# Performance work log

Hardware: AMD Instinct MI355X
Metric: run time of the kernel (lower is better)

Reference implementation:

```python
import jax, jax.numpy as jnp
import numpy as np

N = 50000          # number of parent nodes / neighborhoods
D_IN = 256         # input_size
K = 8              # points decoded per neighborhood
GLOBAL_DIMS = [256, 128, 64]
FC_DIMS = [256, 256, 256]


def _linear_params(key, d_in, d_out):
    kw, kb = jax.random.split(key)
    W = jax.random.normal(kw, (d_in, d_out), dtype=jnp.float32) * 0.05
    b = jax.random.normal(kb, (d_out,), dtype=jnp.float32) * 0.05
    return W, b


def setup_inputs() -> dict:
    key = jax.random.key(0)
    keys = jax.random.split(key, 8)
    inp = {"input_features": jax.random.normal(keys[0], (N, D_IN), dtype=jnp.float32)}
    # global MLP: 256 -> 256 -> 128 -> 64
    d = D_IN
    for i, nb in enumerate(GLOBAL_DIMS):
        W, b = _linear_params(keys[1 + i], d, nb)
        inp[f"Wg{i}"], inp[f"bg{i}"] = W, b
        d = nb
    # neighborhood decoder head: 64 -> K*3
    inp["Wdec"], inp["bdec"] = _linear_params(keys[4], GLOBAL_DIMS[-1], K * 3)
    # per-point MLP: (256 + 64 + 3) -> 256 -> 256 -> 256
    d = D_IN + GLOBAL_DIMS[-1] + 3
    for i, nb in enumerate(FC_DIMS):
        W, b = _linear_params(keys[5 + i], d, nb)
        inp[f"W{i}"], inp[f"b{i}"] = W, b
        d = nb
    return inp


def reference(input_features, Wg0, bg0, Wg1, bg1, Wg2, bg2, Wdec, bdec,
              W0, b0, W1, b1, W2, b2):
    relu = jax.nn.relu
    # global feature MLP on node features: [N, 256] -> [N, 64]
    feats = input_features
    for W, b in ((Wg0, bg0), (Wg1, bg1), (Wg2, bg2)):
        feats = relu(feats @ W + b)
    # neighborhood decoder: K relative 3D points per node -> [N*K, 3]
    relative_points = (feats @ Wdec + bdec).reshape(-1, 3)
    cluster = jnp.repeat(jnp.arange(N, dtype=jnp.int32), K)  # [N*K]
    # gather (duplicate) parent features per decoded point
    nbr_dup = jnp.take(feats, cluster, axis=0)               # [N*K, 64]
    inp_dup = jnp.take(input_features, cluster, axis=0)      # [N*K, 256]
    decoded = jnp.concatenate([inp_dup, nbr_dup, relative_points], axis=1)  # [N*K, 323]
    for W, b in ((W0, b0), (W1, b1), (W2, b2)):
        decoded = relu(decoded @ W + b)
    return relative_points, decoded, cluster
```

## Files before the change

kernel.cpp:

```cpp
#include <hip/hip_runtime.h>
#include <hip/hip_bf16.h>

typedef __attribute__((ext_vector_type(8))) __bf16 bf16x8;
typedef __attribute__((ext_vector_type(4))) float f32x4;
typedef __attribute__((ext_vector_type(4))) unsigned short u16x4;

#define NN 50000
#define TM1 16
#define PNODES 16

#define FEATS_OFF 212992
#define GW_OFF    3412992

__device__ __forceinline__ unsigned short f2bf(float f) {
    unsigned int u = __builtin_bit_cast(unsigned int, f);
    u = (u + 0x7FFFu + ((u >> 16) & 1u)) >> 16;
    return (unsigned short)u;
}
__device__ __forceinline__ float bf2f(unsigned short h) {
    return __builtin_bit_cast(float, (unsigned int)h << 16);
}

__global__ __launch_bounds__(256) void k_prep(
    const float* __restrict__ W0, const float* __restrict__ W1,
    const float* __restrict__ W2,
    const float* __restrict__ Wg0, const float* __restrict__ Wg1,
    const float* __restrict__ Wg2,
    unsigned short* __restrict__ wbf)
{
    int idx = blockIdx.x * 256 + threadIdx.x;
    if (idx < 81920) {
        int n = idx / 320, k = idx - n * 320;
        wbf[idx] = f2bf(W0[(size_t)k * 256 + n]);
    } else if (idx < 147456) {
        int e = idx - 81920;
        int n = e >> 8, k = e & 255;
        wbf[idx] = f2bf(W1[(size_t)k * 256 + n]);
    } else if (idx < 212992) {
        int e = idx - 147456;
        int n = e >> 8, k = e & 255;
        wbf[idx] = f2bf(W2[(size_t)k * 256 + n]);
    } else if (idx < 319488) {
        int e = idx - 212992;
        float v; int oh, ol;
        if (e < 65536) {
            int n = e >> 8, k = e & 255;
            v = Wg0[(size_t)k * 256 + n];
            oh = GW_OFF + e; ol = GW_OFF + 65536 + e;
        } else if (e < 98304) {
            int e2 = e - 65536;
            int n = e2 >> 8, k = e2 & 255;
            v = Wg1[(size_t)k * 128 + n];
            oh = GW_OFF + 131072 + e2; ol = GW_OFF + 163840 + e2;
        } else {
            int e3 = e - 98304;
            int n = e3 >> 7, k = e3 & 127;
            v = Wg2[(size_t)k * 64 + n];
            oh = GW_OFF + 196608 + e3; ol = GW_OFF + 204800 + e3;
        }
        unsigned short h = f2bf(v);
        wbf[oh] = h;
        wbf[ol] = f2bf(v - bf2f(h));
    }
}

__global__ __launch_bounds__(256, 4) void k_global(
    const float* __restrict__ x,
    const float* __restrict__ bg0, const float* __restrict__ bg1,
    const float* __restrict__ bg2,
    const float* __restrict__ Wdec, const float* __restrict__ bdec,
    const unsigned short* __restrict__ gw,
    unsigned short* __restrict__ feats_bf,
    float* __restrict__ out_rel,
    float* __restrict__ out_cluster)
{
    __shared__ __attribute__((aligned(16))) unsigned char smem[37888];
    unsigned short* xh  = (unsigned short*)(smem);
    unsigned short* xl  = (unsigned short*)(smem + 8448);
    unsigned short* q1h = (unsigned short*)(smem);
    unsigned short* q1l = (unsigned short*)(smem + 4352);
    unsigned short* hh  = (unsigned short*)(smem + 16896);
    unsigned short* hl  = (unsigned short*)(smem + 25344);
    float*          g2  = (float*)(smem + 33792);

    const int tid  = threadIdx.x;
    const int lane = tid & 63;
    const int w    = tid >> 6;
    const int quad = lane >> 4;
    const int l15  = lane & 15;
    const int blk  = blockIdx.x;

    {
        const float4* xg = (const float4*)(x + (size_t)blk * TM1 * 256);
        #pragma unroll
        for (int it = 0; it < 4; ++it) {
            int e = tid + it * 256;
            int r = e >> 6, c4 = e & 63;
            float4 v = xg[e];
            u16x4 hv, lv;
            hv[0] = f2bf(v.x); lv[0] = f2bf(v.x - bf2f(hv[0]));
            hv[1] = f2bf(v.y); lv[1] = f2bf(v.y - bf2f(hv[1]));
            hv[2] = f2bf(v.z); lv[2] = f2bf(v.z - bf2f(hv[2]));
            hv[3] = f2bf(v.w); lv[3] = f2bf(v.w - bf2f(hv[3]));
            *(u16x4*)&xh[r * 264 + c4 * 4] = hv;
            *(u16x4*)&xl[r * 264 + c4 * 4] = lv;
        }
    }
    __syncthreads();

    {
        const unsigned short* Wh = gw;
        const unsigned short* Wl = gw + 65536;
        f32x4 acc[4];
        f32x4 z = {0.f, 0.f, 0.f, 0.f};
        #pragma unroll
        for (int t = 0; t < 4; ++t) acc[t] = z;
        for (int ks = 0; ks < 8; ++ks) {
            int k0 = ks * 32 + quad * 8;
            bf16x8 ah = *(const bf16x8*)&xh[l15 * 264 + k0];
            bf16x8 al = *(const bf16x8*)&xl[l15 * 264 + k0];
            #pragma unroll
            for (int t = 0; t < 4; ++t) {
                int n = w * 64 + t * 16 + l15;
                bf16x8 bh = *(const bf16x8*)(Wh + (size_t)n * 256 + k0);
                bf16x8 bl = *(const bf16x8*)(Wl + (size_t)n * 256 + k0);
                acc[t] = __builtin_amdgcn_mfma_f32_16x16x32_bf16(ah, bh, acc[t], 0, 0, 0);
                acc[t] = __builtin_amdgcn_mfma_f32_16x16x32_bf16(al, bh, acc[t], 0, 0, 0);
                acc[t] = __builtin_amdgcn_mfma_f32_16x16x32_bf16(ah, bl, acc[t], 0, 0, 0);
            }
        }
        #pragma unroll
        for (int t = 0; t < 4; ++t) {
            int col = w * 64 + t * 16 + l15;
            float bb = bg0[col];
            #pragma unroll
            for (int r = 0; r < 4; ++r) {
                int row = quad * 4 + r;
                float v = fmaxf(acc[t][r] + bb, 0.f);
                unsigned short h = f2bf(v);
                hh[row * 264 + col] = h;
                hl[row * 264 + col] = f2bf(v - bf2f(h));
            }
        }
    }
    __syncthreads();

    {
        const unsigned short* Wh = gw + 131072;
        const unsigned short* Wl = gw + 163840;
        f32x4 acc[2];
        f32x4 z = {0.f, 0.f, 0.f, 0.f};
        acc[0] = z; acc[1] = z;
        for (int ks = 0; ks < 8; ++ks) {
            int k0 = ks * 32 + quad * 8;
            bf16x8 ah = *(const bf16x8*)&hh[l15 * 264 + k0];
            bf16x8 al = *(const bf16x8*)&hl[l15 * 264 + k0];
            #pragma unroll
            for (int t = 0; t < 2; ++t) {
                int n = w * 32 + t * 16 + l15;
                bf16x8 bh = *(const bf16x8*)(Wh + (size_t)n * 256 + k0);
                bf16x8 bl = *(const bf16x8*)(Wl + (size_t)n * 256 + k0);
                acc[t] = __builtin_amdgcn_mfma_f32_16x16x32_bf16(ah, bh, acc[t], 0, 0, 0);
                acc[t] = __builtin_amdgcn_mfma_f32_16x16x32_bf16(al, bh, acc[t], 0, 0, 0);
                acc[t] = __builtin_amdgcn_mfma_f32_16x16x32_bf16(ah, bl, acc[t], 0, 0, 0);
            }
        }
        #pragma unroll
        for (int t = 0; t < 2; ++t) {
            int col = w * 32 + t * 16 + l15;
            float bb = bg1[col];
            #pragma unroll
            for (int r = 0; r < 4; ++r) {
                int row = quad * 4 + r;
                float v = fmaxf(acc[t][r] + bb, 0.f);
                unsigned short h = f2bf(v);
                q1h[row * 136 + col] = h;
                q1l[row * 136 + col] = f2bf(v - bf2f(h));
            }
        }
    }
    __syncthreads();

    {
        const unsigned short* Wh = gw + 196608;
        const unsigned short* Wl = gw + 204800;
        f32x4 acc = {0.f, 0.f, 0.f, 0.f};
        for (int ks = 0; ks < 4; ++ks) {
            int k0 = ks * 32 + quad * 8;
            bf16x8 ah = *(const bf16x8*)&q1h[l15 * 136 + k0];
            bf16x8 al = *(const bf16x8*)&q1l[l15 * 136 + k0];
            int n = w * 16 + l15;
            bf16x8 bh = *(const bf16x8*)(Wh + (size_t)n * 128 + k0);
            bf16x8 bl = *(const bf16x8*)(Wl + (size_t)n * 128 + k0);
            acc = __builtin_amdgcn_mfma_f32_16x16x32_bf16(ah, bh, acc, 0, 0, 0);
            acc = __builtin_amdgcn_mfma_f32_16x16x32_bf16(al, bh, acc, 0, 0, 0);
            acc = __builtin_amdgcn_mfma_f32_16x16x32_bf16(ah, bl, acc, 0, 0, 0);
        }
        int col = w * 16 + l15;
        float bb = bg2[col];
        #pragma unroll
        for (int r = 0; r < 4; ++r) {
            int row = quad * 4 + r;
            g2[row * 64 + col] = fmaxf(acc[r] + bb, 0.f);
        }
    }
    __syncthreads();

    {
        const float* src = g2 + tid * 4;
        u16x4 p;
        p[0] = f2bf(src[0]); p[1] = f2bf(src[1]);
        p[2] = f2bf(src[2]); p[3] = f2bf(src[3]);
        *(u16x4*)&feats_bf[(size_t)blk * (TM1 * 64) + tid * 4] = p;
    }

    for (int tt = tid; tt < TM1 * 24; tt += 256) {
        int m = tt / 24;
        int c = tt - m * 24;
        float acc = bdec[c];
        for (int i = 0; i < 64; ++i) acc += g2[m * 64 + i] * Wdec[i * 24 + c];
        out_rel[(size_t)blk * (TM1 * 24) + tt] = acc;
    }

    if (tid < TM1 * 8) {
        out_cluster[(size_t)blk * (TM1 * 8) + tid] = (float)(blk * TM1 + (tid >> 3));
    }
}

__global__ __launch_bounds__(512, 4) void k_points(
    const float* __restrict__ x,
    const unsigned short* __restrict__ feats_bf,
    const float* __restrict__ rel_in,
    const unsigned short* __restrict__ wbf,
    const float* __restrict__ W0f,
    const float* __restrict__ b0,
    const float* __restrict__ b1,
    const float* __restrict__ b2,
    float* __restrict__ out_dec)
{
    __shared__ __attribute__((aligned(16))) unsigned char smem[70144];
    unsigned char*  hB   = smem;
    unsigned short* xcat = (unsigned short*)smem;
    float*          sp   = (float*)(smem + 49152);
    float*          w3   = (float*)(smem + 65536);
    float*          rl   = (float*)(smem + 68608);

    const int tid  = threadIdx.x;
    const int lane = tid & 63;
    const int w    = tid >> 6;
    const int wr   = w >> 2;
    const int wc   = w & 3;
    const int quad = lane >> 4;
    const int l15  = lane & 15;
    const int blk  = blockIdx.x;
    const size_t nb = (size_t)blk * PNODES;

    {
        const float4* xg = (const float4*)(x + nb * 256);
        #pragma unroll
        for (int it = 0; it < 2; ++it) {
            int e = tid + it * 512;
            int r = e >> 6, c4 = e & 63;
            float4 v = xg[e];
            u16x4 hv;
            hv[0] = f2bf(v.x); hv[1] = f2bf(v.y);
            hv[2] = f2bf(v.z); hv[3] = f2bf(v.w);
            *(u16x4*)&xcat[r * 336 + c4 * 4] = hv;
        }
        {
            int e = tid * 2;
            int r = e >> 6, c = e & 63;
            *(unsigned int*)&xcat[r * 336 + 256 + c] =
                *(const unsigned int*)&feats_bf[nb * 64 + e];
        }
        for (int e = tid; e < 768; e += 512)
            w3[e] = W0f[(size_t)(320 + (e >> 8)) * 256 + (e & 255)];
        if (tid < 384) rl[tid] = rel_in[nb * 24 + tid];
    }
    __syncthreads();

    {
        const unsigned short* W0t = wbf;
        f32x4 acc[2];
        f32x4 z = {0.f, 0.f, 0.f, 0.f};
        acc[0] = z; acc[1] = z;
        for (int ks = 0; ks < 10; ++ks) {
            int k0 = ks * 32 + quad * 8;
            bf16x8 a = *(const bf16x8*)&xcat[l15 * 336 + k0];
            #pragma unroll
            for (int t = 0; t < 2; ++t) {
                int n = w * 32 + t * 16 + l15;
                bf16x8 b = *(const bf16x8*)(W0t + (size_t)n * 320 + k0);
                acc[t] = __builtin_amdgcn_mfma_f32_16x16x32_bf16(a, b, acc[t], 0, 0, 0);
            }
        }
        #pragma unroll
        for (int t = 0; t < 2; ++t) {
            int col = w * 32 + t * 16 + l15;
            float bb = b0[col];
            #pragma unroll
            for (int r = 0; r < 4; ++r) {
                int row = quad * 4 + r;
                sp[row * 256 + col] = acc[t][r] + bb;
            }
        }
    }
    __syncthreads();

    {
        float4 sv0 = *(const float4*)&sp[(2 * w) * 256 + lane * 4];
        float4 sv1 = *(const float4*)&sp[(2 * w + 1) * 256 + lane * 4];
        float4 wa  = *(const float4*)&w3[lane * 4];
        float4 wb4 = *(const float4*)&w3[256 + lane * 4];
        float4 wc4 = *(const float4*)&w3[512 + lane * 4];
        __syncthreads();
        #pragma unroll
        for (int it = 0; it < 16; ++it) {
            int row  = w * 16 + it;
            int node = 2 * w + (it >> 3);
            int p    = it & 7;
            float4 sv = (it < 8) ? sv0 : sv1;
            float ra = rl[node * 24 + p * 3 + 0];
            float rb = rl[node * 24 + p * 3 + 1];
            float rc = rl[node * 24 + p * 3 + 2];
            float v0 = fmaxf(sv.x + ra * wa.x + rb * wb4.x + rc * wc4.x, 0.f);
            float v1 = fmaxf(sv.y + ra * wa.y + rb * wb4.y + rc * wc4.y, 0.f);
            float v2 = fmaxf(sv.z + ra * wa.z + rb * wb4.z + rc * wc4.z, 0.f);
            float v3 = fmaxf(sv.w + ra * wa.w + rb * wb4.w + rc * wc4.w, 0.f);
            unsigned int lo = (unsigned int)f2bf(v0) | ((unsigned int)f2bf(v1) << 16);
            unsigned int hi = (unsigned int)f2bf(v2) | ((unsigned int)f2bf(v3) << 16);
            uint2 pk; pk.x = lo; pk.y = hi;
            int byteoff = row * 512 +
                ((((lane >> 1) ^ (row & 7)) << 4) | ((lane & 1) << 3));
            *(uint2*)(hB + byteoff) = pk;
        }
    }
    __syncthreads();

    {
        const unsigned short* W1t = wbf + 81920;
        f32x4 acc[4][4];
        f32x4 z = {0.f, 0.f, 0.f, 0.f};
        #pragma unroll
        for (int m = 0; m < 4; ++m)
            #pragma unroll
            for (int t = 0; t < 4; ++t) acc[m][t] = z;
        for (int ks = 0; ks < 8; ++ks) {
            int k0 = ks * 32 + quad * 8;
            int g  = k0 >> 3;
            bf16x8 a[4], b[4];
            #pragma unroll
            for (int m = 0; m < 4; ++m) {
                int row = wr * 64 + m * 16 + l15;
                a[m] = *(const bf16x8*)(hB + row * 512 + ((g ^ (row & 7)) << 4));
            }
            #pragma unroll
            for (int t = 0; t < 4; ++t)
                b[t] = *(const bf16x8*)(W1t + (size_t)(wc * 64 + t * 16 + l15) * 256 + k0);
            #pragma unroll
            for (int m = 0; m < 4; ++m)
                #pragma unroll
                for (int t = 0; t < 4; ++t)
                    acc[m][t] = __builtin_amdgcn_mfma_f32_16x16x32_bf16(a[m], b[t], acc[m][t], 0, 0, 0);
        }
        __syncthreads();
        #pragma unroll
        for (int t = 0; t < 4; ++t) {
            int col = wc * 64 + t * 16 + l15;
            float bb = b1[col];
            #pragma unroll
            for (int m = 0; m < 4; ++m) {
                #pragma unroll
                for (int r = 0; r < 4; ++r) {
                    int row = wr * 64 + m * 16 + quad * 4 + r;
                    int byteoff = row * 512 +
                        ((((col >> 3) ^ (row & 7)) << 4) | ((col & 7) << 1));
                    *(unsigned short*)(hB + byteoff) =
                        f2bf(fmaxf(acc[m][t][r] + bb, 0.f));
                }
            }
        }
    }
    __syncthreads();

    {
        const unsigned short* W2t = wbf + 147456;
        f32x4 acc[4][4];
        f32x4 z = {0.f, 0.f, 0.f, 0.f};
        #pragma unroll
        for (int m = 0; m < 4; ++m)
            #pragma unroll
            for (int t = 0; t < 4; ++t) acc[m][t] = z;
        for (int ks = 0; ks < 8; ++ks) {
            int k0 = ks * 32 + quad * 8;
            int g  = k0 >> 3;
            bf16x8 a[4], b[4];
            #pragma unroll
            for (int m = 0; m < 4; ++m) {
                int row = wr * 64 + m * 16 + l15;
                a[m] = *(const bf16x8*)(hB + row * 512 + ((g ^ (row & 7)) << 4));
            }
            #pragma unroll
            for (int t = 0; t < 4; ++t)
                b[t] = *(const bf16x8*)(W2t + (size_t)(wc * 64 + t * 16 + l15) * 256 + k0);
            #pragma unroll
            for (int m = 0; m < 4; ++m)
                #pragma unroll
                for (int t = 0; t < 4; ++t)
                    acc[m][t] = __builtin_amdgcn_mfma_f32_16x16x32_bf16(a[m], b[t], acc[m][t], 0, 0, 0);
        }
        #pragma unroll
        for (int t = 0; t < 4; ++t) {
            int col = wc * 64 + t * 16 + l15;
            float bb = b2[col];
            #pragma unroll
            for (int m = 0; m < 4; ++m) {
                #pragma unroll
                for (int r = 0; r < 4; ++r) {
                    int row = wr * 64 + m * 16 + quad * 4 + r;
                    out_dec[((size_t)blk * 128 + row) * 256 + col] =
                        fmaxf(acc[m][t][r] + bb, 0.f);
                }
            }
        }
    }
}

extern "C" void kernel_launch(void* const* d_in, const int* in_sizes, int n_in,
                              void* d_out, int out_size, void* d_ws, size_t ws_size,
                              hipStream_t stream) {
    const float* x    = (const float*)d_in[0];
    const float* Wg0  = (const float*)d_in[1];
    const float* bg0  = (const float*)d_in[2];
    const float* Wg1  = (const float*)d_in[3];
    const float* bg1  = (const float*)d_in[4];
    const float* Wg2  = (const float*)d_in[5];
    const float* bg2  = (const float*)d_in[6];
    const float* Wdec = (const float*)d_in[7];
    const float* bdec = (const float*)d_in[8];
    const float* W0   = (const float*)d_in[9];
    const float* b0   = (const float*)d_in[10];
    const float* W1   = (const float*)d_in[11];
    const float* b1   = (const float*)d_in[12];
    const float* W2   = (const float*)d_in[13];
    const float* b2   = (const float*)d_in[14];

    float* out      = (float*)d_out;
    float* out_rel  = out;
    float* out_dec  = out + 1200000;
    float* out_clu  = out + 103600000;

    unsigned short* wbf      = (unsigned short*)d_ws;
    unsigned short* feats_bf = wbf + FEATS_OFF;
    unsigned short* gw       = wbf + GW_OFF;

    k_prep<<<1248, 256, 0, stream>>>(W0, W1, W2, Wg0, Wg1, Wg2, wbf);
    k_global<<<NN / TM1, 256, 0, stream>>>(x, bg0, bg1, bg2, Wdec, bdec, gw,
                                           feats_bf, out_rel, out_clu);
    k_points<<<NN / PNODES, 512, 0, stream>>>(x, feats_bf, out_rel,
                                              wbf, W0, b0, b1, b2, out_dec);
}
```

Baseline: 878.6 us.

## Halve node tiles per block and stage decoder output through LDS for coalesced stores

```diff
diff --git a/kernel.cpp b/kernel.cpp
--- a/kernel.cpp
+++ b/kernel.cpp
@@ -6,8 +6,8 @@
 typedef __attribute__((ext_vector_type(4))) unsigned short u16x4;
 
 #define NN 50000
-#define TM1 16
-#define PNODES 16
+#define GNODES 8
+#define PNODES 8
 
 #define FEATS_OFF 212992
 #define GW_OFF    3412992
@@ -64,7 +64,7 @@
     }
 }
 
-__global__ __launch_bounds__(256, 4) void k_global(
+__global__ __launch_bounds__(256, 6) void k_global(
     const float* __restrict__ x,
     const float* __restrict__ bg0, const float* __restrict__ bg1,
     const float* __restrict__ bg2,
@@ -74,14 +74,14 @@
     float* __restrict__ out_rel,
     float* __restrict__ out_cluster)
 {
-    __shared__ __attribute__((aligned(16))) unsigned char smem[37888];
+    __shared__ __attribute__((aligned(16))) unsigned char smem[18944];
     unsigned short* xh  = (unsigned short*)(smem);
-    unsigned short* xl  = (unsigned short*)(smem + 8448);
+    unsigned short* xl  = (unsigned short*)(smem + 4224);
     unsigned short* q1h = (unsigned short*)(smem);
-    unsigned short* q1l = (unsigned short*)(smem + 4352);
-    unsigned short* hh  = (unsigned short*)(smem + 16896);
-    unsigned short* hl  = (unsigned short*)(smem + 25344);
-    float*          g2  = (float*)(smem + 33792);
+    unsigned short* q1l = (unsigned short*)(smem + 2176);
+    unsigned short* gh  = (unsigned short*)(smem + 8448);
+    unsigned short* gl  = (unsigned short*)(smem + 12672);
+    float*          g2  = (float*)(smem + 16896);
 
     const int tid  = threadIdx.x;
     const int lane = tid & 63;
@@ -89,11 +89,12 @@
     const int quad = lane >> 4;
     const int l15  = lane & 15;
     const int blk  = blockIdx.x;
-
-    {
-        const float4* xg = (const float4*)(x + (size_t)blk * TM1 * 256);
-        #pragma unroll
-        for (int it = 0; it < 4; ++it) {
+    const size_t nb = (size_t)blk * GNODES;
+
+    {
+        const float4* xg = (const float4*)(x + nb * 256);
+        #pragma unroll
+        for (int it = 0; it < 2; ++it) {
             int e = tid + it * 256;
             int r = e >> 6, c4 = e & 63;
             float4 v = xg[e];
@@ -115,10 +116,11 @@
         f32x4 z = {0.f, 0.f, 0.f, 0.f};
         #pragma unroll
         for (int t = 0; t < 4; ++t) acc[t] = z;
+        const int ar = (l15 & 7) * 264;
         for (int ks = 0; ks < 8; ++ks) {
             int k0 = ks * 32 + quad * 8;
-            bf16x8 ah = *(const bf16x8*)&xh[l15 * 264 + k0];
-            bf16x8 al = *(const bf16x8*)&xl[l15 * 264 + k0];
+            bf16x8 ah = *(const bf16x8*)&xh[ar + k0];
+            bf16x8 al = *(const bf16x8*)&xl[ar + k0];
             #pragma unroll
             for (int t = 0; t < 4; ++t) {
                 int n = w * 64 + t * 16 + l15;
@@ -136,10 +138,12 @@
             #pragma unroll
             for (int r = 0; r < 4; ++r) {
                 int row = quad * 4 + r;
-                float v = fmaxf(acc[t][r] + bb, 0.f);
-                unsigned short h = f2bf(v);
-                hh[row * 264 + col] = h;
-                hl[row * 264 + col] = f2bf(v - bf2f(h));
+                if (row < 8) {
+                    float v = fmaxf(acc[t][r] + bb, 0.f);
+                    unsigned short hv = f2bf(v);
+                    gh[row * 264 + col] = hv;
+                    gl[row * 264 + col] = f2bf(v - bf2f(hv));
+                }
             }
         }
     }
@@ -151,10 +155,11 @@
         f32x4 acc[2];
         f32x4 z = {0.f, 0.f, 0.f, 0.f};
         acc[0] = z; acc[1] = z;
+        const int ar = (l15 & 7) * 264;
         for (int ks = 0; ks < 8; ++ks) {
             int k0 = ks * 32 + quad * 8;
-            bf16x8 ah = *(const bf16x8*)&hh[l15 * 264 + k0];
-            bf16x8 al = *(const bf16x8*)&hl[l15 * 264 + k0];
+            bf16x8 ah = *(const bf16x8*)&gh[ar + k0];
+            bf16x8 al = *(const bf16x8*)&gl[ar + k0];
             #pragma unroll
             for (int t = 0; t < 2; ++t) {
                 int n = w * 32 + t * 16 + l15;
@@ -172,10 +177,12 @@
             #pragma unroll
             for (int r = 0; r < 4; ++r) {
                 int row = quad * 4 + r;
-                float v = fmaxf(acc[t][r] + bb, 0.f);
-                unsigned short h = f2bf(v);
-                q1h[row * 136 + col] = h;
-                q1l[row * 136 + col] = f2bf(v - bf2f(h));
+                if (row < 8) {
+                    float v = fmaxf(acc[t][r] + bb, 0.f);
+                    unsigned short hv = f2bf(v);
+                    q1h[row * 136 + col] = hv;
+                    q1l[row * 136 + col] = f2bf(v - bf2f(hv));
+                }
             }
         }
     }
@@ -185,10 +192,11 @@
         const unsigned short* Wh = gw + 196608;
         const unsigned short* Wl = gw + 204800;
         f32x4 acc = {0.f, 0.f, 0.f, 0.f};
+        const int ar = (l15 & 7) * 136;
         for (int ks = 0; ks < 4; ++ks) {
             int k0 = ks * 32 + quad * 8;
-            bf16x8 ah = *(const bf16x8*)&q1h[l15 * 136 + k0];
-            bf16x8 al = *(const bf16x8*)&q1l[l15 * 136 + k0];
+            bf16x8 ah = *(const bf16x8*)&q1h[ar + k0];
+            bf16x8 al = *(const bf16x8*)&q1l[ar + k0];
             int n = w * 16 + l15;
             bf16x8 bh = *(const bf16x8*)(Wh + (size_t)n * 128 + k0);
             bf16x8 bl = *(const bf16x8*)(Wl + (size_t)n * 128 + k0);
@@ -201,33 +209,31 @@
         #pragma unroll
         for (int r = 0; r < 4; ++r) {
             int row = quad * 4 + r;
-            g2[row * 64 + col] = fmaxf(acc[r] + bb, 0.f);
-        }
-    }
-    __syncthreads();
-
-    {
+            if (row < 8) g2[row * 64 + col] = fmaxf(acc[r] + bb, 0.f);
+        }
+    }
+    __syncthreads();
+
+    if (tid < 128) {
         const float* src = g2 + tid * 4;
         u16x4 p;
         p[0] = f2bf(src[0]); p[1] = f2bf(src[1]);
         p[2] = f2bf(src[2]); p[3] = f2bf(src[3]);
-        *(u16x4*)&feats_bf[(size_t)blk * (TM1 * 64) + tid * 4] = p;
-    }
-
-    for (int tt = tid; tt < TM1 * 24; tt += 256) {
-        int m = tt / 24;
-        int c = tt - m * 24;
+        *(u16x4*)&feats_bf[(size_t)blk * 512 + tid * 4] = p;
+    }
+
+    if (tid < 192) {
+        int m = tid / 24, c = tid - m * 24;
         float acc = bdec[c];
         for (int i = 0; i < 64; ++i) acc += g2[m * 64 + i] * Wdec[i * 24 + c];
-        out_rel[(size_t)blk * (TM1 * 24) + tt] = acc;
-    }
-
-    if (tid < TM1 * 8) {
-        out_cluster[(size_t)blk * (TM1 * 8) + tid] = (float)(blk * TM1 + (tid >> 3));
-    }
-}
-
-__global__ __launch_bounds__(512, 4) void k_points(
+        out_rel[(size_t)blk * 192 + tid] = acc;
+    }
+
+    if (tid < 64)
+        out_cluster[(size_t)blk * 64 + tid] = (float)(blk * 8 + (tid >> 3));
+}
+
+__global__ __launch_bounds__(256, 4) void k_points(
     const float* __restrict__ x,
     const unsigned short* __restrict__ feats_bf,
     const float* __restrict__ rel_in,
@@ -238,18 +244,16 @@
     const float* __restrict__ b2,
     float* __restrict__ out_dec)
 {
-    __shared__ __attribute__((aligned(16))) unsigned char smem[70144];
+    __shared__ __attribute__((aligned(16))) unsigned char smem[36608];
     unsigned char*  hB   = smem;
     unsigned short* xcat = (unsigned short*)smem;
-    float*          sp   = (float*)(smem + 49152);
-    float*          w3   = (float*)(smem + 65536);
-    float*          rl   = (float*)(smem + 68608);
+    float*          sp   = (float*)(smem + 24576);
+    float*          w3   = (float*)(smem + 32768);
+    float*          rl   = (float*)(smem + 35840);
 
     const int tid  = threadIdx.x;
     const int lane = tid & 63;
     const int w    = tid >> 6;
-    const int wr   = w >> 2;
-    const int wc   = w & 3;
     const int quad = lane >> 4;
     const int l15  = lane & 15;
     const int blk  = blockIdx.x;
@@ -259,7 +263,7 @@
         const float4* xg = (const float4*)(x + nb * 256);
         #pragma unroll
         for (int it = 0; it < 2; ++it) {
-            int e = tid + it * 512;
+            int e = tid + it * 256;
             int r = e >> 6, c4 = e & 63;
             float4 v = xg[e];
             u16x4 hv;
@@ -273,35 +277,37 @@
             *(unsigned int*)&xcat[r * 336 + 256 + c] =
                 *(const unsigned int*)&feats_bf[nb * 64 + e];
         }
-        for (int e = tid; e < 768; e += 512)
+        for (int e = tid; e < 768; e += 256)
             w3[e] = W0f[(size_t)(320 + (e >> 8)) * 256 + (e & 255)];
-        if (tid < 384) rl[tid] = rel_in[nb * 24 + tid];
+        if (tid < 192) rl[tid] = rel_in[nb * 24 + tid];
     }
     __syncthreads();
 
     {
         const unsigned short* W0t = wbf;
-        f32x4 acc[2];
+        f32x4 acc[4];
         f32x4 z = {0.f, 0.f, 0.f, 0.f};
-        acc[0] = z; acc[1] = z;
+        #pragma unroll
+        for (int t = 0; t < 4; ++t) acc[t] = z;
+        const int ar = (lane & 7) * 336;
         for (int ks = 0; ks < 10; ++ks) {
             int k0 = ks * 32 + quad * 8;
-            bf16x8 a = *(const bf16x8*)&xcat[l15 * 336 + k0];
-            #pragma unroll
-            for (int t = 0; t < 2; ++t) {
-                int n = w * 32 + t * 16 + l15;
+            bf16x8 a = *(const bf16x8*)&xcat[ar + k0];
+            #pragma unroll
+            for (int t = 0; t < 4; ++t) {
+                int n = w * 64 + t * 16 + l15;
                 bf16x8 b = *(const bf16x8*)(W0t + (size_t)n * 320 + k0);
                 acc[t] = __builtin_amdgcn_mfma_f32_16x16x32_bf16(a, b, acc[t], 0, 0, 0);
             }
         }
         #pragma unroll
-        for (int t = 0; t < 2; ++t) {
-            int col = w * 32 + t * 16 + l15;
+        for (int t = 0; t < 4; ++t) {
+            int col = w * 64 + t * 16 + l15;
             float bb = b0[col];
             #pragma unroll
             for (int r = 0; r < 4; ++r) {
                 int row = quad * 4 + r;
-                sp[row * 256 + col] = acc[t][r] + bb;
+                if (row < 8) sp[row * 256 + col] = acc[t][r] + bb;
             }
         }
     }
@@ -351,12 +357,12 @@
             bf16x8 a[4], b[4];
             #pragma unroll
             for (int m = 0; m < 4; ++m) {
-                int row = wr * 64 + m * 16 + l15;
+                int row = m * 16 + l15;
                 a[m] = *(const bf16x8*)(hB + row * 512 + ((g ^ (row & 7)) << 4));
             }
             #pragma unroll
             for (int t = 0; t < 4; ++t)
-                b[t] = *(const bf16x8*)(W1t + (size_t)(wc * 64 + t * 16 + l15) * 256 + k0);
+                b[t] = *(const bf16x8*)(W1t + (size_t)(w * 64 + t * 16 + l15) * 256 + k0);
             #pragma unroll
             for (int m = 0; m < 4; ++m)
                 #pragma unroll
@@ -366,13 +372,13 @@
         __syncthreads();
         #pragma unroll
         for (int t = 0; t < 4; ++t) {
-            int col = wc * 64 + t * 16 + l15;
+            int col = w * 64 + t * 16 + l15;
             float bb = b1[col];
             #pragma unroll
             for (int m = 0; m < 4; ++m) {
                 #pragma unroll
                 for (int r = 0; r < 4; ++r) {
-                    int row = wr * 64 + m * 16 + quad * 4 + r;
+                    int row = m * 16 + quad * 4 + r;
                     int byteoff = row * 512 +
                         ((((col >> 3) ^ (row & 7)) << 4) | ((col & 7) << 1));
                     *(unsigned short*)(hB + byteoff) =
@@ -397,30 +403,49 @@
             bf16x8 a[4], b[4];
             #pragma unroll
             for (int m = 0; m < 4; ++m) {
-                int row = wr * 64 + m * 16 + l15;
+                int row = m * 16 + l15;
                 a[m] = *(const bf16x8*)(hB + row * 512 + ((g ^ (row & 7)) << 4));
             }
             #pragma unroll
             for (int t = 0; t < 4; ++t)
-                b[t] = *(const bf16x8*)(W2t + (size_t)(wc * 64 + t * 16 + l15) * 256 + k0);
+                b[t] = *(const bf16x8*)(W2t + (size_t)(w * 64 + t * 16 + l15) * 256 + k0);
             #pragma unroll
             for (int m = 0; m < 4; ++m)
                 #pragma unroll
                 for (int t = 0; t < 4; ++t)
                     acc[m][t] = __builtin_amdgcn_mfma_f32_16x16x32_bf16(a[m], b[t], acc[m][t], 0, 0, 0);
         }
-        #pragma unroll
-        for (int t = 0; t < 4; ++t) {
-            int col = wc * 64 + t * 16 + l15;
-            float bb = b2[col];
-            #pragma unroll
-            for (int m = 0; m < 4; ++m) {
+        __syncthreads();
+
+        float* ofw = (float*)(hB + (size_t)w * 8192);
+        float bb[4];
+        #pragma unroll
+        for (int t = 0; t < 4; ++t) bb[t] = b2[w * 64 + t * 16 + l15];
+        #pragma unroll
+        for (int half = 0; half < 2; ++half) {
+            #pragma unroll
+            for (int mm = 0; mm < 2; ++mm) {
+                int m = half * 2 + mm;
                 #pragma unroll
-                for (int r = 0; r < 4; ++r) {
-                    int row = wr * 64 + m * 16 + quad * 4 + r;
-                    out_dec[((size_t)blk * 128 + row) * 256 + col] =
-                        fmaxf(acc[m][t][r] + bb, 0.f);
+                for (int t = 0; t < 4; ++t) {
+                    int c = t * 16 + l15;
+                    int csw = c ^ (quad << 3);
+                    #pragma unroll
+                    for (int r = 0; r < 4; ++r) {
+                        int rloc = mm * 16 + quad * 4 + r;
+                        ofw[rloc * 64 + csw] = fmaxf(acc[m][t][r] + bb[t], 0.f);
+                    }
                 }
+            }
+            #pragma unroll
+            for (int i = 0; i < 8; ++i) {
+                int e = lane + i * 64;
+                int rloc = e >> 4, gc = e & 15;
+                f32x4 v = *(const f32x4*)&ofw[rloc * 64 +
+                    ((gc * 4) ^ ((((rloc >> 2) & 3)) << 3))];
+                int row = half * 32 + rloc;
+                *(f32x4*)&out_dec[((size_t)blk * 64 + row) * 256 +
+                                  w * 64 + gc * 4] = v;
             }
         }
     }
@@ -455,8 +480,8 @@
     unsigned short* gw       = wbf + GW_OFF;
 
     k_prep<<<1248, 256, 0, stream>>>(W0, W1, W2, Wg0, Wg1, Wg2, wbf);
-    k_global<<<NN / TM1, 256, 0, stream>>>(x, bg0, bg1, bg2, Wdec, bdec, gw,
-                                           feats_bf, out_rel, out_clu);
-    k_points<<<NN / PNODES, 512, 0, stream>>>(x, feats_bf, out_rel,
+    k_global<<<NN / GNODES, 256, 0, stream>>>(x, bg0, bg1, bg2, Wdec, bdec, gw,
+                                              feats_bf, out_rel, out_clu);
+    k_points<<<NN / PNODES, 256, 0, stream>>>(x, feats_bf, out_rel,
                                               wbf, W0, b0, b1, b2, out_dec);
 }
```

After: 1.037 ms. +18.0%, slower.

## Shrink global-MLP LDS footprint and register-prefetch weight fragments across K steps

Applied to the files above, without the earlier changes.

```diff
diff --git a/kernel.cpp b/kernel.cpp
--- a/kernel.cpp
+++ b/kernel.cpp
@@ -64,7 +64,7 @@
     }
 }
 
-__global__ __launch_bounds__(256, 4) void k_global(
+__global__ __launch_bounds__(256, 6) void k_global(
     const float* __restrict__ x,
     const float* __restrict__ bg0, const float* __restrict__ bg1,
     const float* __restrict__ bg2,
@@ -74,14 +74,12 @@
     float* __restrict__ out_rel,
     float* __restrict__ out_cluster)
 {
-    __shared__ __attribute__((aligned(16))) unsigned char smem[37888];
-    unsigned short* xh  = (unsigned short*)(smem);
-    unsigned short* xl  = (unsigned short*)(smem + 8448);
-    unsigned short* q1h = (unsigned short*)(smem);
-    unsigned short* q1l = (unsigned short*)(smem + 4352);
-    unsigned short* hh  = (unsigned short*)(smem + 16896);
-    unsigned short* hl  = (unsigned short*)(smem + 25344);
-    float*          g2  = (float*)(smem + 33792);
+    __shared__ __attribute__((aligned(16))) unsigned char smem[25600];
+    unsigned short* bufA = (unsigned short*)(smem);
+    unsigned short* bufB = (unsigned short*)(smem + 8448);
+    unsigned short* q1h  = (unsigned short*)(smem + 16896);
+    unsigned short* q1l  = (unsigned short*)(smem + 21248);
+    float*          g2   = (float*)(smem + 16896);
 
     const int tid  = threadIdx.x;
     const int lane = tid & 63;
@@ -102,33 +100,42 @@
             hv[1] = f2bf(v.y); lv[1] = f2bf(v.y - bf2f(hv[1]));
             hv[2] = f2bf(v.z); lv[2] = f2bf(v.z - bf2f(hv[2]));
             hv[3] = f2bf(v.w); lv[3] = f2bf(v.w - bf2f(hv[3]));
-            *(u16x4*)&xh[r * 264 + c4 * 4] = hv;
-            *(u16x4*)&xl[r * 264 + c4 * 4] = lv;
-        }
-    }
-    __syncthreads();
-
+            *(u16x4*)&bufA[r * 264 + c4 * 4] = hv;
+            *(u16x4*)&bufB[r * 264 + c4 * 4] = lv;
+        }
+    }
+    __syncthreads();
+
+    f32x4 accL0[4];
     {
         const unsigned short* Wh = gw;
         const unsigned short* Wl = gw + 65536;
-        f32x4 acc[4];
         f32x4 z = {0.f, 0.f, 0.f, 0.f};
         #pragma unroll
-        for (int t = 0; t < 4; ++t) acc[t] = z;
+        for (int t = 0; t < 4; ++t) accL0[t] = z;
+        #pragma unroll
         for (int ks = 0; ks < 8; ++ks) {
             int k0 = ks * 32 + quad * 8;
-            bf16x8 ah = *(const bf16x8*)&xh[l15 * 264 + k0];
-            bf16x8 al = *(const bf16x8*)&xl[l15 * 264 + k0];
+            bf16x8 ah = *(const bf16x8*)&bufA[l15 * 264 + k0];
+            bf16x8 al = *(const bf16x8*)&bufB[l15 * 264 + k0];
+            bf16x8 bh[4], bl[4];
             #pragma unroll
             for (int t = 0; t < 4; ++t) {
                 int n = w * 64 + t * 16 + l15;
-                bf16x8 bh = *(const bf16x8*)(Wh + (size_t)n * 256 + k0);
-                bf16x8 bl = *(const bf16x8*)(Wl + (size_t)n * 256 + k0);
-                acc[t] = __builtin_amdgcn_mfma_f32_16x16x32_bf16(ah, bh, acc[t], 0, 0, 0);
-                acc[t] = __builtin_amdgcn_mfma_f32_16x16x32_bf16(al, bh, acc[t], 0, 0, 0);
-                acc[t] = __builtin_amdgcn_mfma_f32_16x16x32_bf16(ah, bl, acc[t], 0, 0, 0);
-            }
-        }
+                bh[t] = *(const bf16x8*)(Wh + (size_t)n * 256 + k0);
+                bl[t] = *(const bf16x8*)(Wl + (size_t)n * 256 + k0);
+            }
+            #pragma unroll
+            for (int t = 0; t < 4; ++t) {
+                accL0[t] = __builtin_amdgcn_mfma_f32_16x16x32_bf16(ah, bh[t], accL0[t], 0, 0, 0);
+                accL0[t] = __builtin_amdgcn_mfma_f32_16x16x32_bf16(al, bh[t], accL0[t], 0, 0, 0);
+                accL0[t] = __builtin_amdgcn_mfma_f32_16x16x32_bf16(ah, bl[t], accL0[t], 0, 0, 0);
+            }
+        }
+    }
+    __syncthreads();
+
+    {
         #pragma unroll
         for (int t = 0; t < 4; ++t) {
             int col = w * 64 + t * 16 + l15;
@@ -136,10 +143,10 @@
             #pragma unroll
             for (int r = 0; r < 4; ++r) {
                 int row = quad * 4 + r;
-                float v = fmaxf(acc[t][r] + bb, 0.f);
+                float v = fmaxf(accL0[t][r] + bb, 0.f);
                 unsigned short h = f2bf(v);
-                hh[row * 264 + col] = h;
-                hl[row * 264 + col] = f2bf(v - bf2f(h));
+                bufA[row * 264 + col] = h;
+                bufB[row * 264 + col] = f2bf(v - bf2f(h));
             }
         }
     }
@@ -151,18 +158,23 @@
         f32x4 acc[2];
         f32x4 z = {0.f, 0.f, 0.f, 0.f};
         acc[0] = z; acc[1] = z;
+        #pragma unroll
         for (int ks = 0; ks < 8; ++ks) {
             int k0 = ks * 32 + quad * 8;
-            bf16x8 ah = *(const bf16x8*)&hh[l15 * 264 + k0];
-            bf16x8 al = *(const bf16x8*)&hl[l15 * 264 + k0];
+            bf16x8 ah = *(const bf16x8*)&bufA[l15 * 264 + k0];
+            bf16x8 al = *(const bf16x8*)&bufB[l15 * 264 + k0];
+            bf16x8 bh[2], bl[2];
             #pragma unroll
             for (int t = 0; t < 2; ++t) {
                 int n = w * 32 + t * 16 + l15;
-                bf16x8 bh = *(const bf16x8*)(Wh + (size_t)n * 256 + k0);
-                bf16x8 bl = *(const bf16x8*)(Wl + (size_t)n * 256 + k0);
-                acc[t] = __builtin_amdgcn_mfma_f32_16x16x32_bf16(ah, bh, acc[t], 0, 0, 0);
-                acc[t] = __builtin_amdgcn_mfma_f32_16x16x32_bf16(al, bh, acc[t], 0, 0, 0);
-                acc[t] = __builtin_amdgcn_mfma_f32_16x16x32_bf16(ah, bl, acc[t], 0, 0, 0);
+                bh[t] = *(const bf16x8*)(Wh + (size_t)n * 256 + k0);
+                bl[t] = *(const bf16x8*)(Wl + (size_t)n * 256 + k0);
+            }
+            #pragma unroll
+            for (int t = 0; t < 2; ++t) {
+                acc[t] = __builtin_amdgcn_mfma_f32_16x16x32_bf16(ah, bh[t], acc[t], 0, 0, 0);
+                acc[t] = __builtin_amdgcn_mfma_f32_16x16x32_bf16(al, bh[t], acc[t], 0, 0, 0);
+                acc[t] = __builtin_amdgcn_mfma_f32_16x16x32_bf16(ah, bl[t], acc[t], 0, 0, 0);
             }
         }
         #pragma unroll
@@ -181,10 +193,13 @@
     }
     __syncthreads();
 
+    f32x4 accL2;
     {
         const unsigned short* Wh = gw + 196608;
         const unsigned short* Wl = gw + 204800;
-        f32x4 acc = {0.f, 0.f, 0.f, 0.f};
+        f32x4 z = {0.f, 0.f, 0.f, 0.f};
+        accL2 = z;
+        #pragma unroll
         for (int ks = 0; ks < 4; ++ks) {
             int k0 = ks * 32 + quad * 8;
             bf16x8 ah = *(const bf16x8*)&q1h[l15 * 136 + k0];
@@ -192,16 +207,20 @@
             int n = w * 16 + l15;
             bf16x8 bh = *(const bf16x8*)(Wh + (size_t)n * 128 + k0);
             bf16x8 bl = *(const bf16x8*)(Wl + (size_t)n * 128 + k0);
-            acc = __builtin_amdgcn_mfma_f32_16x16x32_bf16(ah, bh, acc, 0, 0, 0);
-            acc = __builtin_amdgcn_mfma_f32_16x16x32_bf16(al, bh, acc, 0, 0, 0);
-            acc = __builtin_amdgcn_mfma_f32_16x16x32_bf16(ah, bl, acc, 0, 0, 0);
-        }
+            accL2 = __builtin_amdgcn_mfma_f32_16x16x32_bf16(ah, bh, accL2, 0, 0, 0);
+            accL2 = __builtin_amdgcn_mfma_f32_16x16x32_bf16(al, bh, accL2, 0, 0, 0);
+            accL2 = __builtin_amdgcn_mfma_f32_16x16x32_bf16(ah, bl, accL2, 0, 0, 0);
+        }
+    }
+    __syncthreads();
+
+    {
         int col = w * 16 + l15;
         float bb = bg2[col];
         #pragma unroll
         for (int r = 0; r < 4; ++r) {
             int row = quad * 4 + r;
-            g2[row * 64 + col] = fmaxf(acc[r] + bb, 0.f);
+            g2[row * 64 + col] = fmaxf(accL2[r] + bb, 0.f);
         }
     }
     __syncthreads();
@@ -284,14 +303,25 @@
         f32x4 acc[2];
         f32x4 z = {0.f, 0.f, 0.f, 0.f};
         acc[0] = z; acc[1] = z;
+        bf16x8 bcur[2], bnxt[2];
+        #pragma unroll
+        for (int t = 0; t < 2; ++t)
+            bcur[t] = *(const bf16x8*)(W0t + (size_t)(w * 32 + t * 16 + l15) * 320 + quad * 8);
+        #pragma unroll
         for (int ks = 0; ks < 10; ++ks) {
             int k0 = ks * 32 + quad * 8;
             bf16x8 a = *(const bf16x8*)&xcat[l15 * 336 + k0];
-            #pragma unroll
-            for (int t = 0; t < 2; ++t) {
-                int n = w * 32 + t * 16 + l15;
-                bf16x8 b = *(const bf16x8*)(W0t + (size_t)n * 320 + k0);
-                acc[t] = __builtin_amdgcn_mfma_f32_16x16x32_bf16(a, b, acc[t], 0, 0, 0);
+            if (ks < 9) {
+                #pragma unroll
+                for (int t = 0; t < 2; ++t)
+                    bnxt[t] = *(const bf16x8*)(W0t + (size_t)(w * 32 + t * 16 + l15) * 320 + k0 + 32);
+            }
+            #pragma unroll
+            for (int t = 0; t < 2; ++t)
+                acc[t] = __builtin_amdgcn_mfma_f32_16x16x32_bf16(a, bcur[t], acc[t], 0, 0, 0);
+            if (ks < 9) {
+                #pragma unroll
+                for (int t = 0; t < 2; ++t) bcur[t] = bnxt[t];
             }
         }
         #pragma unroll
@@ -345,23 +375,34 @@
         for (int m = 0; m < 4; ++m)
             #pragma unroll
             for (int t = 0; t < 4; ++t) acc[m][t] = z;
+        bf16x8 bcur[4], bnxt[4];
+        #pragma unroll
+        for (int t = 0; t < 4; ++t)
+            bcur[t] = *(const bf16x8*)(W1t + (size_t)(wc * 64 + t * 16 + l15) * 256 + quad * 8);
+        #pragma unroll
         for (int ks = 0; ks < 8; ++ks) {
             int k0 = ks * 32 + quad * 8;
             int g  = k0 >> 3;
-            bf16x8 a[4], b[4];
+            bf16x8 a[4];
             #pragma unroll
             for (int m = 0; m < 4; ++m) {
                 int row = wr * 64 + m * 16 + l15;
                 a[m] = *(const bf16x8*)(hB + row * 512 + ((g ^ (row & 7)) << 4));
             }
-            #pragma unroll
-            for (int t = 0; t < 4; ++t)
-                b[t] = *(const bf16x8*)(W1t + (size_t)(wc * 64 + t * 16 + l15) * 256 + k0);
+            if (ks < 7) {
+                #pragma unroll
+                for (int t = 0; t < 4; ++t)
+                    bnxt[t] = *(const bf16x8*)(W1t + (size_t)(wc * 64 + t * 16 + l15) * 256 + k0 + 32);
+            }
             #pragma unroll
             for (int m = 0; m < 4; ++m)
                 #pragma unroll
                 for (int t = 0; t < 4; ++t)
-                    acc[m][t] = __builtin_amdgcn_mfma_f32_16x16x32_bf16(a[m], b[t], acc[m][t], 0, 0, 0);
+                    acc[m][t] = __builtin_amdgcn_mfma_f32_16x16x32_bf16(a[m], bcur[t], acc[m][t], 0, 0, 0);
+            if (ks < 7) {
+                #pragma unroll
+                for (int t = 0; t < 4; ++t) bcur[t] = bnxt[t];
+            }
         }
         __syncthreads();
         #pragma unroll
@@ -391,23 +432,34 @@
         for (int m = 0; m < 4; ++m)
             #pragma unroll
             for (int t = 0; t < 4; ++t) acc[m][t] = z;
+        bf16x8 bcur[4], bnxt[4];
+        #pragma unroll
+        for (int t = 0; t < 4; ++t)
+            bcur[t] = *(const bf16x8*)(W2t + (size_t)(wc * 64 + t * 16 + l15) * 256 + quad * 8);
+        #pragma unroll
         for (int ks = 0; ks < 8; ++ks) {
             int k0 = ks * 32 + quad * 8;
             int g  = k0 >> 3;
-            bf16x8 a[4], b[4];
+            bf16x8 a[4];
             #pragma unroll
             for (int m = 0; m < 4; ++m) {
                 int row = wr * 64 + m * 16 + l15;
                 a[m] = *(const bf16x8*)(hB + row * 512 + ((g ^ (row & 7)) << 4));
             }
-            #pragma unroll
-            for (int t = 0; t < 4; ++t)
-                b[t] = *(const bf16x8*)(W2t + (size_t)(wc * 64 + t * 16 + l15) * 256 + k0);
+            if (ks < 7) {
+                #pragma unroll
+                for (int t = 0; t < 4; ++t)
+                    bnxt[t] = *(const bf16x8*)(W2t + (size_t)(wc * 64 + t * 16 + l15) * 256 + k0 + 32);
+            }
             #pragma unroll
             for (int m = 0; m < 4; ++m)
                 #pragma unroll
                 for (int t = 0; t < 4; ++t)
-                    acc[m][t] = __builtin_amdgcn_mfma_f32_16x16x32_bf16(a[m], b[t], acc[m][t], 0, 0, 0);
+                    acc[m][t] = __builtin_amdgcn_mfma_f32_16x16x32_bf16(a[m], bcur[t], acc[m][t], 0, 0, 0);
+            if (ks < 7) {
+                #pragma unroll
+                for (int t = 0; t < 4; ++t) bcur[t] = bnxt[t];
+            }
         }
         #pragma unroll
         for (int t = 0; t < 4; ++t) {
```

Result: no change. 876.5 us (-0.2%).
